# Kernel optimization log

Measured on AMD Instinct MI355X. Metric: run time of the kernel, lower is better.

Reference implementation:

```python
import jax, jax.numpy as jnp
import numpy as np

B, L1, V, E, H, Z = 16, 257, 32000, 256, 256, 256


def _lstm_layer(x, Wih, Whh, bih, bhh):
    # x: [B, T, E_in]; PyTorch gate order i, f, g, o
    b, H_ = x.shape[0], Whh.shape[1]

    def step(carry, xt):
        h, c = carry
        gates = xt @ Wih.T + h @ Whh.T + (bih + bhh)
        i, f, g, o = jnp.split(gates, 4, axis=-1)
        c = jax.nn.sigmoid(f) * c + jax.nn.sigmoid(i) * jnp.tanh(g)
        h = jax.nn.sigmoid(o) * jnp.tanh(c)
        return (h, c), h

    h0 = jnp.zeros((b, H_), x.dtype)
    _, hs = jax.lax.scan(step, (h0, h0), jnp.swapaxes(x, 0, 1))
    return jnp.swapaxes(hs, 0, 1)  # [B, T, H]


def setup_inputs() -> dict:
    key = jax.random.key(0)
    ks = jax.random.split(key, 16)
    s = 1.0 / np.sqrt(H)
    inp = {
        "z": jax.random.normal(ks[0], (B, Z), jnp.float32),
        "target_seq": jax.random.randint(ks[1], (B, L1), 0, V),
        "emb": jax.random.normal(ks[2], (V, E), jnp.float32) * 0.02,
        "Wg": jax.random.normal(ks[3], (H, Z), jnp.float32) * s,
        "bg": jax.random.normal(ks[4], (H,), jnp.float32) * s,
        "Wb": jax.random.normal(ks[5], (H, Z), jnp.float32) * s,
        "bb": jax.random.normal(ks[6], (H,), jnp.float32) * s,
        "W_ih0": jax.random.normal(ks[7], (4 * H, E), jnp.float32) * s,
        "W_hh0": jax.random.normal(ks[8], (4 * H, H), jnp.float32) * s,
        "b_ih0": jax.random.normal(ks[9], (4 * H,), jnp.float32) * s,
        "b_hh0": jax.random.normal(ks[10], (4 * H,), jnp.float32) * s,
        "W_ih1": jax.random.normal(ks[11], (4 * H, H), jnp.float32) * s,
        "W_hh1": jax.random.normal(ks[12], (4 * H, H), jnp.float32) * s,
        "b_ih1": jax.random.normal(ks[13], (4 * H,), jnp.float32) * s,
        "b_hh1": jax.random.normal(ks[14], (4 * H,), jnp.float32) * s,
        "W_out": jax.random.normal(ks[15], (V, H), jnp.float32) * s,
        "b_out": jnp.zeros((V,), jnp.float32),
    }
    return inp


def reference(z, target_seq, emb, Wg, bg, Wb, bb, W_ih0, W_hh0, b_ih0, b_hh0,
              W_ih1, W_hh1, b_ih1, b_hh1, W_out, b_out):
    # Teacher-forcing branch (eval mode: dropout = identity).
    emb_t = emb.at[0].set(0.0)  # padding_idx=0
    gamma = (z @ Wg.T + bg)[:, None, :]  # [B,1,H]
    beta = (z @ Wb.T + bb)[:, None, :]
    x = emb_t[target_seq[:, :-1]]  # [B, L, E]
    h1 = _lstm_layer(x, W_ih0, W_hh0, b_ih0, b_hh0)
    h2 = _lstm_layer(h1, W_ih1, W_hh1, b_ih1, b_hh1)
    filmed = gamma * h2 + beta  # [B, L, H]
    logits = filmed @ W_out.T + b_out  # [B, L, V]
    return logits
```

## Files before the change

### kernel.cpp

```cpp
#include <hip/hip_runtime.h>
#include <stdint.h>


#define B_  16
#define T_  256
#define H_  256
#define V_  32000
#define G4  1024

#define LTPB 512
#define FSTR 32

typedef unsigned short u16;
typedef unsigned long long u64;
typedef __attribute__((ext_vector_type(8))) short  short8;
typedef __attribute__((ext_vector_type(4))) short  short4v;
typedef __attribute__((ext_vector_type(4))) float  f32x4;

static __device__ __forceinline__ float bf2f(u16 u) {
  uint32_t i = ((uint32_t)u) << 16;
  return __builtin_bit_cast(float, i);
}
static __device__ __forceinline__ u16 f2bf(float f) {
  uint32_t i = __builtin_bit_cast(uint32_t, f);
  uint32_t lsb = (i >> 16) & 1u;
  i += 0x7fffu + lsb;
  return (u16)(i >> 16);
}
static __device__ __forceinline__ float sigf(float x) {
  return 1.0f / (1.0f + __expf(-x));
}
static __device__ __forceinline__ float tanhfast(float x) {
  return 1.0f - 2.0f / (1.0f + __expf(2.0f * x));
}

static __device__ __forceinline__ uint32_t f32_to_e4m3(float f) {
  uint32_t u = __builtin_bit_cast(uint32_t, f);
  uint32_t s = (u >> 24) & 0x80u;
  uint32_t mag = u & 0x7fffffffu;
  if (mag >= 0x43E00000u) return s | 0x7Eu;
  if (mag < 0x3C800000u) {
    float af = __builtin_bit_cast(float, mag);
    int q = (int)rintf(af * 512.0f);
    if (q >= 8) return s | 0x08u;
    return s | (uint32_t)q;
  }
  uint32_t lsb = (mag >> 20) & 1u;
  mag += 0x7ffffu + lsb;
  int e = (int)(mag >> 23) - 120;
  uint32_t m3 = (mag >> 20) & 7u;
  if (e >= 16) return s | 0x7Eu;
  return s | ((uint32_t)e << 3) | m3;
}


__global__ void k_convert(const float* __restrict__ src, u16* __restrict__ dst, int n) {
  int i = blockIdx.x * blockDim.x + threadIdx.x;
  int stride = gridDim.x * blockDim.x;
  for (; i < n; i += stride) dst[i] = f2bf(src[i]);
}

__global__ void k_addbias(const float* __restrict__ a, const float* __restrict__ b,
                          float* __restrict__ dst, int n) {
  int i = blockIdx.x * blockDim.x + threadIdx.x;
  if (i < n) dst[i] = a[i] + b[i];
}

__global__ void k_zeroi(int* __restrict__ p, int n) {
  int i = blockIdx.x * blockDim.x + threadIdx.x;
  if (i < n) p[i] = 0;
}

__global__ void k_packWg(const float* __restrict__ Whh, u16* __restrict__ pk) {
  int i = blockIdx.x * blockDim.x + threadIdx.x;
  int lane = i & 63;
  int fb = (i >> 6) & 15;
  int w  = i >> 10;
  int cb = fb >> 3, ks = fb & 7;
  int row = 512 + w * 32 + cb * 16 + (lane & 15);
  int kb  = ks * 32 + (lane >> 4) * 8;
  const float* src = Whh + (size_t)row * 256 + kb;
  short8 v;
  #pragma unroll
  for (int j = 0; j < 8; j++) v[j] = (short)f2bf(src[j]);
  *(short8*)(pk + (size_t)i * 8) = v;
}

__global__ void k_packW8(const float* __restrict__ Whh, u64* __restrict__ pk) {
  int i = blockIdx.x * blockDim.x + threadIdx.x;
  int lane = i & 63;
  int fo = (i >> 6) % 48;
  int w  = (i >> 6) / 48;
  int g8 = fo >> 4, cb = (fo >> 3) & 1, ks = fo & 7;
  int base = (g8 == 0) ? 0 : (g8 == 1 ? 256 : 768);
  int row = base + w * 32 + cb * 16 + (lane & 15);
  int kb  = ks * 32 + (lane >> 4) * 8;
  const float* src = Whh + (size_t)row * 256 + kb;
  u64 p = 0;
  #pragma unroll
  for (int j = 0; j < 8; j++)
    p |= ((u64)f32_to_e4m3(src[j])) << (8 * j);
  pk[i] = p;
}

__global__ void k_film(const float* __restrict__ z,
                       const float* __restrict__ Wg, const float* __restrict__ bg,
                       const float* __restrict__ Wb, const float* __restrict__ bb,
                       float* __restrict__ gamma, float* __restrict__ beta) {
  int tid = blockIdx.x * blockDim.x + threadIdx.x;
  int which = tid >> 12;
  int o = tid & 4095;
  int b = o >> 8, h = o & 255;
  const float* W  = which ? Wb : Wg;
  const float* bi = which ? bb : bg;
  float acc = bi[h];
  const float* zr = z + b * 256;
  const float* wr = W + h * 256;
  #pragma unroll 8
  for (int k = 0; k < 256; k++) acc += zr[k] * wr[k];
  (which ? beta : gamma)[o] = acc;
}

__global__ void k_gather(const int* __restrict__ seq, const float* __restrict__ emb,
                         u16* __restrict__ xb) {
  int i = blockIdx.x * blockDim.x + threadIdx.x;
  int n = B_ * T_ * (H_ / 4);
  if (i >= n) return;
  int e4 = i & 63;
  int bt = i >> 6;
  int t = bt & 255, b = bt >> 8;
  int row = seq[b * 257 + t];
  short4v p;
  if (row == 0) {
    p[0] = 0; p[1] = 0; p[2] = 0; p[3] = 0;
  } else {
    const f32x4 v = *(const f32x4*)(emb + (size_t)row * 256 + e4 * 4);
    p[0] = (short)f2bf(v[0]); p[1] = (short)f2bf(v[1]);
    p[2] = (short)f2bf(v[2]); p[3] = (short)f2bf(v[3]);
  }
  *(short4v*)(xb + (size_t)bt * 256 + e4 * 4) = p;
}


__global__ __launch_bounds__(256) void k_gemm_bt(
    const u16* __restrict__ A, const u16* __restrict__ Bm,
    const float* __restrict__ bias, float* __restrict__ C,
    int M, int N, int K, int permX) {
  __shared__ u16 sA[128 * 40];
  __shared__ u16 sB[128 * 40];
  const int tid  = threadIdx.x;
  const int lane = tid & 63;
  const int wv   = tid >> 6;
  const int wr   = wv >> 1, wc = wv & 1;
  const int m0 = blockIdx.y * 128, n0 = blockIdx.x * 128;
  const int rr = tid >> 2;
  const int cc = (tid & 3) * 8;

  f32x4 acc[4][4];
  #pragma unroll
  for (int m = 0; m < 4; m++)
    #pragma unroll
    for (int n = 0; n < 4; n++) acc[m][n] = (f32x4){0.f, 0.f, 0.f, 0.f};

  for (int ks = 0; ks < K; ks += 32) {
    short8 va0 = *(const short8*)(A  + (size_t)(m0 + rr)      * K + ks + cc);
    short8 va1 = *(const short8*)(A  + (size_t)(m0 + rr + 64) * K + ks + cc);
    short8 vb0 = *(const short8*)(Bm + (size_t)(n0 + rr)      * K + ks + cc);
    short8 vb1 = *(const short8*)(Bm + (size_t)(n0 + rr + 64) * K + ks + cc);
    __syncthreads();
    *(short8*)&sA[(rr)      * 40 + cc] = va0;
    *(short8*)&sA[(rr + 64) * 40 + cc] = va1;
    *(short8*)&sB[(rr)      * 40 + cc] = vb0;
    *(short8*)&sB[(rr + 64) * 40 + cc] = vb1;
    __syncthreads();
    const int kc = (lane >> 4) * 8;
    short8 af[4], bfr[4];
    #pragma unroll
    for (int m = 0; m < 4; m++)
      af[m] = *(const short8*)&sA[(wr * 64 + m * 16 + (lane & 15)) * 40 + kc];
    #pragma unroll
    for (int n = 0; n < 4; n++)
      bfr[n] = *(const short8*)&sB[(wc * 64 + n * 16 + (lane & 15)) * 40 + kc];
    #pragma unroll
    for (int m = 0; m < 4; m++)
      #pragma unroll
      for (int n = 0; n < 4; n++)
        acc[m][n] = __builtin_amdgcn_mfma_f32_16x16x32_bf16(af[m], bfr[n], acc[m][n], 0, 0, 0);
  }

  #pragma unroll
  for (int m = 0; m < 4; m++) {
    int row = m0 + wr * 64 + m * 16 + ((lane >> 4) << 2);
    #pragma unroll
    for (int n = 0; n < 4; n++) {
      int col = n0 + wc * 64 + n * 16 + (lane & 15);
      float bv = bias[col];
      int ocol = col;
      if (permX) {
        int g = col >> 8, r = col & 255;
        ocol = (r >> 5) * 128 + (r & 15) * 8 + g * 2 + ((r >> 4) & 1);
      }
      #pragma unroll
      for (int i = 0; i < 4; i++)
        C[(size_t)(row + i) * N + ocol] = acc[m][n][i] + bv;
    }
  }
}


static __device__ __forceinline__ void lstm_role(
    const float* __restrict__ Xpre, const u16* __restrict__ WpkG,
    const u64* __restrict__ Wpk8, u16* __restrict__ outb,
    const float* __restrict__ gamma, const float* __restrict__ beta,
    int mode, int s, int* flagOut, const int* flagIn,
    u16 (*hbuf)[256], u64 (*h8buf)[32]) {
  const int tid  = threadIdx.x;
  const int lane = tid & 63;
  const int w    = tid >> 6;
  const int l15  = lane & 15;
  const int lhi  = lane >> 4;

  short8 wgm[16];
  {
    const u16* bp = WpkG + ((size_t)(w * 16) * 64 + lane) * 8;
    #pragma unroll
    for (int f = 0; f < 16; ++f)
      wgm[f] = *(const short8*)(bp + (size_t)f * 512);
  }
  u64 w8r[48];
  {
    const u64* p8 = Wpk8 + (size_t)(w * 48) * 64 + lane;
    #pragma unroll
    for (int f = 0; f < 48; ++f)
      w8r[f] = p8[(size_t)f * 64];
  }

  const int col0 = w * 32 + l15;
  const int col1 = col0 + 16;
  float cs0 = 0.f, cs1 = 0.f;
  float gm0 = 1.f, gm1 = 1.f, bt0 = 0.f, bt1 = 0.f;
  if (mode) {
    gm0 = gamma[s * 256 + col0]; bt0 = beta[s * 256 + col0];
    gm1 = gamma[s * 256 + col1]; bt1 = beta[s * 256 + col1];
  }

  if (flagIn) {
    if (tid == 0) {
      while (__hip_atomic_load(flagIn, __ATOMIC_RELAXED,
                               __HIP_MEMORY_SCOPE_AGENT) < 1) { }
    }
    __syncthreads();
    __builtin_amdgcn_fence(__ATOMIC_ACQUIRE, "agent");
  }

  const float* xptr = Xpre + (size_t)s * T_ * 1024 + (size_t)(w * 16 + l15) * 8;

  f32x4 xa = *(const f32x4*)(xptr);
  f32x4 xg = *(const f32x4*)(xptr + 4);
  {
    float cn0 = sigf(xa[2]) * cs0 + sigf(xa[0]) * tanhfast(xg[0]);
    float hn0 = sigf(xg[2]) * tanhfast(cn0);
    cs0 = cn0;
    float cn1 = sigf(xa[3]) * cs1 + sigf(xa[1]) * tanhfast(xg[1]);
    float hn1 = sigf(xg[3]) * tanhfast(cn1);
    cs1 = cn1;
    u16 h0 = f2bf(hn0), h1 = f2bf(hn1);
    if (lhi == 0) {
      hbuf[0][col0] = h0;
      hbuf[0][col1] = h1;
      ((uint8_t*)h8buf[0])[col0] = (uint8_t)f32_to_e4m3(hn0);
      ((uint8_t*)h8buf[0])[col1] = (uint8_t)f32_to_e4m3(hn1);
      outb[(size_t)(s * T_) * 256 + col0] = mode ? f2bf(gm0 * hn0 + bt0) : h0;
      outb[(size_t)(s * T_) * 256 + col1] = mode ? f2bf(gm1 * hn1 + bt1) : h1;
    }
  }
  asm volatile("s_waitcnt lgkmcnt(0)" ::: "memory");
  __builtin_amdgcn_sched_barrier(0);
  __builtin_amdgcn_s_barrier();
  __builtin_amdgcn_sched_barrier(0);

  xa = *(const f32x4*)(xptr + 1024);
  xg = *(const f32x4*)(xptr + 1024 + 4);

  for (int t = 1; t < T_; ++t) {
    if (flagIn && (t & 15) == 15 && (t + 1) < T_) {
      const int need = ((t + 1) >> 4) + 1;
      if (tid == 0) {
        while (__hip_atomic_load(flagIn, __ATOMIC_RELAXED,
                                 __HIP_MEMORY_SCOPE_AGENT) < need) { }
      }
      __syncthreads();
      __builtin_amdgcn_fence(__ATOMIC_ACQUIRE, "agent");
    }

    const float* xn = xptr + (size_t)((t + 1 < T_) ? t + 1 : t) * 1024;
    f32x4 na = *(const f32x4*)(xn);
    f32x4 ng = *(const f32x4*)(xn + 4);

    const u16* hrd  = hbuf[(t + 1) & 1];
    const u64* h8rd = h8buf[(t + 1) & 1];

    f32x4 aI[2], aF[2], aG[2], aO[2];
    #pragma unroll
    for (int i = 0; i < 2; ++i) {
      aI[i] = (f32x4){0.f, 0.f, 0.f, 0.f};
      aF[i] = (f32x4){0.f, 0.f, 0.f, 0.f};
      aG[i] = (f32x4){0.f, 0.f, 0.f, 0.f};
      aO[i] = (f32x4){0.f, 0.f, 0.f, 0.f};
    }
    #pragma unroll
    for (int ks = 0; ks < 8; ++ks) {
      short8 a  = *(const short8*)&hrd[ks * 32 + lhi * 8];
      u64    a8 = h8rd[ks * 4 + lhi];
      aG[0] = __builtin_amdgcn_mfma_f32_16x16x32_bf16(a, wgm[ks],     aG[0], 0, 0, 0);
      aG[1] = __builtin_amdgcn_mfma_f32_16x16x32_bf16(a, wgm[8 + ks], aG[1], 0, 0, 0);
      aI[0] = __builtin_amdgcn_mfma_f32_16x16x32_fp8_fp8((long)a8, (long)w8r[ks],      aI[0], 0, 0, 0);
      aI[1] = __builtin_amdgcn_mfma_f32_16x16x32_fp8_fp8((long)a8, (long)w8r[8 + ks],  aI[1], 0, 0, 0);
      aF[0] = __builtin_amdgcn_mfma_f32_16x16x32_fp8_fp8((long)a8, (long)w8r[16 + ks], aF[0], 0, 0, 0);
      aF[1] = __builtin_amdgcn_mfma_f32_16x16x32_fp8_fp8((long)a8, (long)w8r[24 + ks], aF[1], 0, 0, 0);
      aO[0] = __builtin_amdgcn_mfma_f32_16x16x32_fp8_fp8((long)a8, (long)w8r[32 + ks], aO[0], 0, 0, 0);
      aO[1] = __builtin_amdgcn_mfma_f32_16x16x32_fp8_fp8((long)a8, (long)w8r[40 + ks], aO[1], 0, 0, 0);
    }

    float iv0 = aI[0][0] + xa[0], iv1 = aI[1][0] + xa[1];
    float fv0 = aF[0][0] + xa[2], fv1 = aF[1][0] + xa[3];
    float gv0 = aG[0][0] + xg[0], gv1 = aG[1][0] + xg[1];
    float ov0 = aO[0][0] + xg[2], ov1 = aO[1][0] + xg[3];

    float cn0 = sigf(fv0) * cs0 + sigf(iv0) * tanhfast(gv0);
    float hn0 = sigf(ov0) * tanhfast(cn0);
    cs0 = cn0;
    float cn1 = sigf(fv1) * cs1 + sigf(iv1) * tanhfast(gv1);
    float hn1 = sigf(ov1) * tanhfast(cn1);
    cs1 = cn1;

    u16 h0 = f2bf(hn0), h1 = f2bf(hn1);
    if (lhi == 0) {
      hbuf[t & 1][col0] = h0;
      hbuf[t & 1][col1] = h1;
      ((uint8_t*)h8buf[t & 1])[col0] = (uint8_t)f32_to_e4m3(hn0);
      ((uint8_t*)h8buf[t & 1])[col1] = (uint8_t)f32_to_e4m3(hn1);
      outb[((size_t)(s * T_ + t)) * 256 + col0] = mode ? f2bf(gm0 * hn0 + bt0) : h0;
      outb[((size_t)(s * T_ + t)) * 256 + col1] = mode ? f2bf(gm1 * hn1 + bt1) : h1;
    }

    if (flagOut && (t & 15) == 15) {
      __syncthreads();
      if (tid == 0) {
        __builtin_amdgcn_fence(__ATOMIC_RELEASE, "agent");
        __hip_atomic_store(flagOut, t + 1, __ATOMIC_RELAXED,
                           __HIP_MEMORY_SCOPE_AGENT);
      }
    } else {
      asm volatile("s_waitcnt lgkmcnt(0)" ::: "memory");
      __builtin_amdgcn_sched_barrier(0);
      __builtin_amdgcn_s_barrier();
      __builtin_amdgcn_sched_barrier(0);
    }

    xa = na;
    xg = ng;
  }
}

static __device__ __forceinline__ void xg_role(
    const u16* __restrict__ h1b, const u16* __restrict__ Wih1b,
    const float* __restrict__ b11, float* __restrict__ X1,
    int s, const int* flagA, int* flagB) {
  const int tid  = threadIdx.x;
  const int lane = tid & 63;
  const int w    = tid >> 6;
  const int l15  = lane & 15;
  const int lhi  = lane >> 4;

  for (int tc = 0; tc < 16; ++tc) {
    const int need = (tc + 1) * 16;
    if (tid == 0) {
      while (__hip_atomic_load(flagA, __ATOMIC_RELAXED,
                               __HIP_MEMORY_SCOPE_AGENT) < need) { }
    }
    __syncthreads();
    __builtin_amdgcn_fence(__ATOMIC_ACQUIRE, "agent");

    const int t0 = tc * 16;
    short8 afr[8];
    #pragma unroll
    for (int ks = 0; ks < 8; ++ks)
      afr[ks] = *(const short8*)(h1b + ((size_t)(s * T_ + t0 + l15)) * 256 + ks * 32 + lhi * 8);

    #pragma unroll
    for (int nt = 0; nt < 8; ++nt) {
      const int colb = w * 128 + nt * 16 + l15;
      f32x4 acc = (f32x4){0.f, 0.f, 0.f, 0.f};
      const u16* bp = Wih1b + (size_t)colb * 256 + lhi * 8;
      #pragma unroll
      for (int ks = 0; ks < 8; ++ks) {
        short8 bf = *(const short8*)(bp + ks * 32);
        acc = __builtin_amdgcn_mfma_f32_16x16x32_bf16(afr[ks], bf, acc, 0, 0, 0);
      }
      const int g = colb >> 8, r = colb & 255;
      const int ocol = (r >> 5) * 128 + (r & 15) * 8 + g * 2 + ((r >> 4) & 1);
      const float bv = b11[colb];
      #pragma unroll
      for (int i = 0; i < 4; ++i) {
        int trow = t0 + lhi * 4 + i;
        X1[((size_t)(s * T_ + trow)) * 1024 + ocol] = acc[i] + bv;
      }
    }

    __syncthreads();
    if (tid == 0) {
      __builtin_amdgcn_fence(__ATOMIC_RELEASE, "agent");
      __hip_atomic_store(flagB, tc + 1, __ATOMIC_RELAXED,
                         __HIP_MEMORY_SCOPE_AGENT);
    }
  }
}

__global__ __launch_bounds__(LTPB, 2) void k_fused(
    const float* __restrict__ X0, float* __restrict__ X1,
    const u16* __restrict__ WpG0, const u64* __restrict__ Wp80,
    const u16* __restrict__ WpG1, const u64* __restrict__ Wp81,
    const u16* __restrict__ Wih1b, const float* __restrict__ b11,
    u16* __restrict__ h1b, u16* __restrict__ filmb,
    const float* __restrict__ gamma, const float* __restrict__ beta,
    int* __restrict__ flagA, int* __restrict__ flagB) {
  __shared__ u16 hbuf[2][256];
  __shared__ u64 h8buf[2][32];
  const int role = blockIdx.x >> 4;
  const int s    = blockIdx.x & 15;
  if (role == 0) {
    lstm_role(X0, WpG0, Wp80, h1b, gamma, beta, 0, s,
              &flagA[s * FSTR], nullptr, hbuf, h8buf);
  } else if (role == 1) {
    xg_role(h1b, Wih1b, b11, X1, s, &flagA[s * FSTR], &flagB[s * FSTR]);
  } else {
    lstm_role(X1, WpG1, Wp81, filmb, gamma, beta, 1, s,
              nullptr, &flagB[s * FSTR], hbuf, h8buf);
  }
}


extern "C" void kernel_launch(void* const* d_in, const int* in_sizes, int n_in,
                              void* d_out, int out_size, void* d_ws, size_t ws_size,
                              hipStream_t stream) {
  const float* z    = (const float*)d_in[0];
  const int*   seq  = (const int*)  d_in[1];
  const float* emb  = (const float*)d_in[2];
  const float* Wg   = (const float*)d_in[3];
  const float* bg   = (const float*)d_in[4];
  const float* Wb   = (const float*)d_in[5];
  const float* bb   = (const float*)d_in[6];
  const float* Wih0 = (const float*)d_in[7];
  const float* Whh0 = (const float*)d_in[8];
  const float* bih0 = (const float*)d_in[9];
  const float* bhh0 = (const float*)d_in[10];
  const float* Wih1 = (const float*)d_in[11];
  const float* Whh1 = (const float*)d_in[12];
  const float* bih1 = (const float*)d_in[13];
  const float* bhh1 = (const float*)d_in[14];
  const float* Wout = (const float*)d_in[15];
  const float* bout = (const float*)d_in[16];

  char* ws = (char*)d_ws;
  size_t off = 0;
  auto take = [&](size_t bytes) -> char* {
    char* p = ws + off;
    off = (off + bytes + 255) & ~(size_t)255;
    return p;
  };
  float* gamma  = (float*)take(B_ * H_ * 4);
  float* beta   = (float*)take(B_ * H_ * 4);
  float* b01    = (float*)take(G4 * 4);
  float* b11    = (float*)take(G4 * 4);
  u16*   Wih0b  = (u16*)  take((size_t)G4 * H_ * 2);
  u16*   Wih1b  = (u16*)  take((size_t)G4 * H_ * 2);
  u16*   WpG0   = (u16*)  take((size_t)8 * 16 * 64 * 8 * 2);
  u64*   Wp80   = (u64*)  take((size_t)8 * 48 * 64 * 8);
  u16*   WpG1   = (u16*)  take((size_t)8 * 16 * 64 * 8 * 2);
  u64*   Wp81   = (u64*)  take((size_t)8 * 48 * 64 * 8);
  u16*   Woutb  = (u16*)  take((size_t)V_ * H_ * 2);
  u16*   xb     = (u16*)  take((size_t)B_ * T_ * H_ * 2);
  float* X0     = (float*)take((size_t)B_ * T_ * G4 * 4);
  float* X1     = (float*)take((size_t)B_ * T_ * G4 * 4);
  u16*   h1b    = (u16*)  take((size_t)B_ * T_ * H_ * 2);
  u16*   filmb  = (u16*)  take((size_t)B_ * T_ * H_ * 2);
  int*   flagA  = (int*)  take(B_ * FSTR * 4);
  int*   flagB  = (int*)  take(B_ * FSTR * 4);
  (void)ws_size; (void)in_sizes; (void)n_in; (void)out_size;

  k_convert<<<256, 256, 0, stream>>>(Wih0, Wih0b, G4 * H_);
  k_convert<<<256, 256, 0, stream>>>(Wih1, Wih1b, G4 * H_);
  k_convert<<<1024, 256, 0, stream>>>(Wout, Woutb, V_ * H_);
  k_packWg<<<32, 256, 0, stream>>>(Whh0, WpG0);
  k_packW8<<<96, 256, 0, stream>>>(Whh0, Wp80);
  k_packWg<<<32, 256, 0, stream>>>(Whh1, WpG1);
  k_packW8<<<96, 256, 0, stream>>>(Whh1, Wp81);
  k_addbias<<<4, 256, 0, stream>>>(bih0, bhh0, b01, G4);
  k_addbias<<<4, 256, 0, stream>>>(bih1, bhh1, b11, G4);
  k_zeroi<<<4, 256, 0, stream>>>(flagA, 2 * B_ * FSTR);
  k_film<<<32, 256, 0, stream>>>(z, Wg, bg, Wb, bb, gamma, beta);
  k_gather<<<1024, 256, 0, stream>>>(seq, emb, xb);

  k_gemm_bt<<<dim3(G4 / 128, (B_ * T_) / 128), 256, 0, stream>>>(
      xb, Wih0b, b01, X0, B_ * T_, G4, H_, 1);

  k_fused<<<48, LTPB, 0, stream>>>(X0, X1, WpG0, Wp80, WpG1, Wp81,
                                   Wih1b, b11, h1b, filmb, gamma, beta,
                                   flagA, flagB);

  k_gemm_bt<<<dim3(V_ / 128, (B_ * T_) / 128), 256, 0, stream>>>(
      filmb, Woutb, bout, (float*)d_out, B_ * T_, V_, H_, 0);
}
```

Measured before the change: 746.6 us.

## Fuse input projection and vocab GEMM into persistent pipelined LSTM kernel

Removes the two standalone GEMM launches. The layer-0 input projection and the vocabulary projection now run as extra roles inside the fused persistent kernel, linked to the LSTM roles through per-sequence flags. The vocab blocks spin on layer-1 progress and compute 64-row by 128-column output tiles as soon as the filmed hidden states are ready, so the large output GEMM overlaps the sequential recurrence. This relies on all 512 blocks being co-resident, because of the spin-waits. The vocab tile is smaller than the old 128x128 GEMM tile and the B operand is loaded straight from global memory, which may lower GEMM efficiency.

```diff
diff --git a/kernel.cpp b/kernel.cpp
--- a/kernel.cpp
+++ b/kernel.cpp
@@ -10,6 +10,8 @@
 
 #define LTPB 512
 #define FSTR 32
+#define NVW  448
+#define SASTR 264
 
 typedef unsigned short u16;
 typedef unsigned long long u64;
@@ -139,72 +141,6 @@
     p[2] = (short)f2bf(v[2]); p[3] = (short)f2bf(v[3]);
   }
   *(short4v*)(xb + (size_t)bt * 256 + e4 * 4) = p;
-}
-
-
-__global__ __launch_bounds__(256) void k_gemm_bt(
-    const u16* __restrict__ A, const u16* __restrict__ Bm,
-    const float* __restrict__ bias, float* __restrict__ C,
-    int M, int N, int K, int permX) {
-  __shared__ u16 sA[128 * 40];
-  __shared__ u16 sB[128 * 40];
-  const int tid  = threadIdx.x;
-  const int lane = tid & 63;
-  const int wv   = tid >> 6;
-  const int wr   = wv >> 1, wc = wv & 1;
-  const int m0 = blockIdx.y * 128, n0 = blockIdx.x * 128;
-  const int rr = tid >> 2;
-  const int cc = (tid & 3) * 8;
-
-  f32x4 acc[4][4];
-  #pragma unroll
-  for (int m = 0; m < 4; m++)
-    #pragma unroll
-    for (int n = 0; n < 4; n++) acc[m][n] = (f32x4){0.f, 0.f, 0.f, 0.f};
-
-  for (int ks = 0; ks < K; ks += 32) {
-    short8 va0 = *(const short8*)(A  + (size_t)(m0 + rr)      * K + ks + cc);
-    short8 va1 = *(const short8*)(A  + (size_t)(m0 + rr + 64) * K + ks + cc);
-    short8 vb0 = *(const short8*)(Bm + (size_t)(n0 + rr)      * K + ks + cc);
-    short8 vb1 = *(const short8*)(Bm + (size_t)(n0 + rr + 64) * K + ks + cc);
-    __syncthreads();
-    *(short8*)&sA[(rr)      * 40 + cc] = va0;
-    *(short8*)&sA[(rr + 64) * 40 + cc] = va1;
-    *(short8*)&sB[(rr)      * 40 + cc] = vb0;
-    *(short8*)&sB[(rr + 64) * 40 + cc] = vb1;
-    __syncthreads();
-    const int kc = (lane >> 4) * 8;
-    short8 af[4], bfr[4];
-    #pragma unroll
-    for (int m = 0; m < 4; m++)
-      af[m] = *(const short8*)&sA[(wr * 64 + m * 16 + (lane & 15)) * 40 + kc];
-    #pragma unroll
-    for (int n = 0; n < 4; n++)
-      bfr[n] = *(const short8*)&sB[(wc * 64 + n * 16 + (lane & 15)) * 40 + kc];
-    #pragma unroll
-    for (int m = 0; m < 4; m++)
-      #pragma unroll
-      for (int n = 0; n < 4; n++)
-        acc[m][n] = __builtin_amdgcn_mfma_f32_16x16x32_bf16(af[m], bfr[n], acc[m][n], 0, 0, 0);
-  }
-
-  #pragma unroll
-  for (int m = 0; m < 4; m++) {
-    int row = m0 + wr * 64 + m * 16 + ((lane >> 4) << 2);
-    #pragma unroll
-    for (int n = 0; n < 4; n++) {
-      int col = n0 + wc * 64 + n * 16 + (lane & 15);
-      float bv = bias[col];
-      int ocol = col;
-      if (permX) {
-        int g = col >> 8, r = col & 255;
-        ocol = (r >> 5) * 128 + (r & 15) * 8 + g * 2 + ((r >> 4) & 1);
-      }
-      #pragma unroll
-      for (int i = 0; i < 4; i++)
-        C[(size_t)(row + i) * N + ocol] = acc[m][n][i] + bv;
-    }
-  }
 }
 
 
@@ -363,10 +299,10 @@
   }
 }
 
-static __device__ __forceinline__ void xg_role(
-    const u16* __restrict__ h1b, const u16* __restrict__ Wih1b,
-    const float* __restrict__ b11, float* __restrict__ X1,
-    int s, const int* flagA, int* flagB) {
+static __device__ __forceinline__ void proj_role(
+    const u16* __restrict__ src, const u16* __restrict__ Wb_,
+    const float* __restrict__ bias, float* __restrict__ dst,
+    int s, const int* flagIn, int* flagOut) {
   const int tid  = threadIdx.x;
   const int lane = tid & 63;
   const int w    = tid >> 6;
@@ -374,25 +310,27 @@
   const int lhi  = lane >> 4;
 
   for (int tc = 0; tc < 16; ++tc) {
-    const int need = (tc + 1) * 16;
-    if (tid == 0) {
-      while (__hip_atomic_load(flagA, __ATOMIC_RELAXED,
-                               __HIP_MEMORY_SCOPE_AGENT) < need) { }
-    }
-    __syncthreads();
-    __builtin_amdgcn_fence(__ATOMIC_ACQUIRE, "agent");
+    if (flagIn) {
+      const int need = (tc + 1) * 16;
+      if (tid == 0) {
+        while (__hip_atomic_load(flagIn, __ATOMIC_RELAXED,
+                                 __HIP_MEMORY_SCOPE_AGENT) < need) { }
+      }
+      __syncthreads();
+      __builtin_amdgcn_fence(__ATOMIC_ACQUIRE, "agent");
+    }
 
     const int t0 = tc * 16;
     short8 afr[8];
     #pragma unroll
     for (int ks = 0; ks < 8; ++ks)
-      afr[ks] = *(const short8*)(h1b + ((size_t)(s * T_ + t0 + l15)) * 256 + ks * 32 + lhi * 8);
+      afr[ks] = *(const short8*)(src + ((size_t)(s * T_ + t0 + l15)) * 256 + ks * 32 + lhi * 8);
 
     #pragma unroll
     for (int nt = 0; nt < 8; ++nt) {
       const int colb = w * 128 + nt * 16 + l15;
       f32x4 acc = (f32x4){0.f, 0.f, 0.f, 0.f};
-      const u16* bp = Wih1b + (size_t)colb * 256 + lhi * 8;
+      const u16* bp = Wb_ + (size_t)colb * 256 + lhi * 8;
       #pragma unroll
       for (int ks = 0; ks < 8; ++ks) {
         short8 bf = *(const short8*)(bp + ks * 32);
@@ -400,43 +338,116 @@
       }
       const int g = colb >> 8, r = colb & 255;
       const int ocol = (r >> 5) * 128 + (r & 15) * 8 + g * 2 + ((r >> 4) & 1);
-      const float bv = b11[colb];
+      const float bv = bias[colb];
       #pragma unroll
       for (int i = 0; i < 4; ++i) {
         int trow = t0 + lhi * 4 + i;
-        X1[((size_t)(s * T_ + trow)) * 1024 + ocol] = acc[i] + bv;
+        dst[((size_t)(s * T_ + trow)) * 1024 + ocol] = acc[i] + bv;
       }
     }
 
     __syncthreads();
     if (tid == 0) {
       __builtin_amdgcn_fence(__ATOMIC_RELEASE, "agent");
-      __hip_atomic_store(flagB, tc + 1, __ATOMIC_RELAXED,
+      __hip_atomic_store(flagOut, tc + 1, __ATOMIC_RELAXED,
                          __HIP_MEMORY_SCOPE_AGENT);
     }
   }
 }
 
+static __device__ __forceinline__ void vocab_role(
+    const u16* __restrict__ filmb, const u16* __restrict__ Wo,
+    const float* __restrict__ bout, float* __restrict__ out,
+    const int* __restrict__ flagC, int wid, u16* __restrict__ sA) {
+  const int tid  = threadIdx.x;
+  const int lane = tid & 63;
+  const int w    = tid >> 6;
+  const int l15  = lane & 15;
+  const int lhi  = lane >> 4;
+
+  for (int n = wid; n < 16000; n += NVW) {
+    const int q   = n / 4000;
+    const int rem = n - q * 4000;
+    const int s   = rem / 250;
+    const int nt  = rem - s * 250;
+    const int need = q * 64 + 64;
+    if (tid == 0) {
+      while (__hip_atomic_load(&flagC[s * FSTR], __ATOMIC_RELAXED,
+                               __HIP_MEMORY_SCOPE_AGENT) < need) { }
+    }
+    __syncthreads();
+    __builtin_amdgcn_fence(__ATOMIC_ACQUIRE, "agent");
+
+    const int m0 = s * 256 + q * 64;
+    const int n0 = nt * 128;
+
+    {
+      const int r = tid >> 3, c = tid & 7;
+      const u16* srow = filmb + (size_t)(m0 + r) * 256 + c * 8;
+      #pragma unroll
+      for (int it = 0; it < 4; ++it)
+        *(short8*)&sA[r * SASTR + c * 8 + it * 64] = *(const short8*)(srow + it * 64);
+    }
+    __syncthreads();
+
+    const int colb = n0 + w * 16 + l15;
+    short8 bfr[8];
+    #pragma unroll
+    for (int ks = 0; ks < 8; ++ks)
+      bfr[ks] = *(const short8*)(Wo + (size_t)colb * 256 + ks * 32 + lhi * 8);
+
+    f32x4 acc[4];
+    #pragma unroll
+    for (int mi = 0; mi < 4; ++mi) acc[mi] = (f32x4){0.f, 0.f, 0.f, 0.f};
+    #pragma unroll
+    for (int ks = 0; ks < 8; ++ks) {
+      #pragma unroll
+      for (int mi = 0; mi < 4; ++mi) {
+        short8 a = *(const short8*)&sA[(mi * 16 + l15) * SASTR + ks * 32 + lhi * 8];
+        acc[mi] = __builtin_amdgcn_mfma_f32_16x16x32_bf16(a, bfr[ks], acc[mi], 0, 0, 0);
+      }
+    }
+
+    const float bv = bout[colb];
+    #pragma unroll
+    for (int mi = 0; mi < 4; ++mi)
+      #pragma unroll
+      for (int i = 0; i < 4; ++i)
+        out[(size_t)(m0 + mi * 16 + lhi * 4 + i) * V_ + colb] = acc[mi][i] + bv;
+  }
+}
+
 __global__ __launch_bounds__(LTPB, 2) void k_fused(
-    const float* __restrict__ X0, float* __restrict__ X1,
+    const u16* __restrict__ xb, float* __restrict__ X0, float* __restrict__ X1,
     const u16* __restrict__ WpG0, const u64* __restrict__ Wp80,
     const u16* __restrict__ WpG1, const u64* __restrict__ Wp81,
+    const u16* __restrict__ Wih0b, const float* __restrict__ b01,
     const u16* __restrict__ Wih1b, const float* __restrict__ b11,
-    u16* __restrict__ h1b, u16* __restrict__ filmb,
+    const u16* __restrict__ Woutb, const float* __restrict__ bout,
+    u16* __restrict__ h1b, u16* __restrict__ filmb, float* __restrict__ out,
     const float* __restrict__ gamma, const float* __restrict__ beta,
-    int* __restrict__ flagA, int* __restrict__ flagB) {
+    int* __restrict__ flagX, int* __restrict__ flagA,
+    int* __restrict__ flagB, int* __restrict__ flagC) {
   __shared__ u16 hbuf[2][256];
   __shared__ u64 h8buf[2][32];
-  const int role = blockIdx.x >> 4;
-  const int s    = blockIdx.x & 15;
-  if (role == 0) {
+  __shared__ u16 sA[64 * SASTR];
+
+  const int bid = blockIdx.x;
+  if (bid < 16) {
+    proj_role(xb, Wih0b, b01, X0, bid, nullptr, &flagX[bid * FSTR]);
+  } else if (bid < 32) {
+    const int s = bid - 16;
     lstm_role(X0, WpG0, Wp80, h1b, gamma, beta, 0, s,
-              &flagA[s * FSTR], nullptr, hbuf, h8buf);
-  } else if (role == 1) {
-    xg_role(h1b, Wih1b, b11, X1, s, &flagA[s * FSTR], &flagB[s * FSTR]);
+              &flagA[s * FSTR], &flagX[s * FSTR], hbuf, h8buf);
+  } else if (bid < 48) {
+    const int s = bid - 32;
+    proj_role(h1b, Wih1b, b11, X1, s, &flagA[s * FSTR], &flagB[s * FSTR]);
+  } else if (bid < 64) {
+    const int s = bid - 48;
+    lstm_role(X1, WpG1, Wp81, filmb, gamma, beta, 1, s,
+              &flagC[s * FSTR], &flagB[s * FSTR], hbuf, h8buf);
   } else {
-    lstm_role(X1, WpG1, Wp81, filmb, gamma, beta, 1, s,
-              nullptr, &flagB[s * FSTR], hbuf, h8buf);
+    vocab_role(filmb, Woutb, bout, out, flagC, bid - 64, sA);
   }
 }
 
@@ -485,8 +496,10 @@
   float* X1     = (float*)take((size_t)B_ * T_ * G4 * 4);
   u16*   h1b    = (u16*)  take((size_t)B_ * T_ * H_ * 2);
   u16*   filmb  = (u16*)  take((size_t)B_ * T_ * H_ * 2);
+  int*   flagX  = (int*)  take(B_ * FSTR * 4);
   int*   flagA  = (int*)  take(B_ * FSTR * 4);
   int*   flagB  = (int*)  take(B_ * FSTR * 4);
+  int*   flagC  = (int*)  take(B_ * FSTR * 4);
   (void)ws_size; (void)in_sizes; (void)n_in; (void)out_size;
 
   k_convert<<<256, 256, 0, stream>>>(Wih0, Wih0b, G4 * H_);
@@ -498,17 +511,12 @@
   k_packW8<<<96, 256, 0, stream>>>(Whh1, Wp81);
   k_addbias<<<4, 256, 0, stream>>>(bih0, bhh0, b01, G4);
   k_addbias<<<4, 256, 0, stream>>>(bih1, bhh1, b11, G4);
-  k_zeroi<<<4, 256, 0, stream>>>(flagA, 2 * B_ * FSTR);
+  k_zeroi<<<8, 256, 0, stream>>>(flagX, 4 * B_ * FSTR);
   k_film<<<32, 256, 0, stream>>>(z, Wg, bg, Wb, bb, gamma, beta);
   k_gather<<<1024, 256, 0, stream>>>(seq, emb, xb);
 
-  k_gemm_bt<<<dim3(G4 / 128, (B_ * T_) / 128), 256, 0, stream>>>(
-      xb, Wih0b, b01, X0, B_ * T_, G4, H_, 1);
-
-  k_fused<<<48, LTPB, 0, stream>>>(X0, X1, WpG0, Wp80, WpG1, Wp81,
-                                   Wih1b, b11, h1b, filmb, gamma, beta,
-                                   flagA, flagB);
-
-  k_gemm_bt<<<dim3(V_ / 128, (B_ * T_) / 128), 256, 0, stream>>>(
-      filmb, Woutb, bout, (float*)d_out, B_ * T_, V_, H_, 0);
-}
+  k_fused<<<64 + NVW, LTPB, 0, stream>>>(
+      xb, X0, X1, WpG0, Wp80, WpG1, Wp81, Wih0b, b01, Wih1b, b11,
+      Woutb, bout, h1b, filmb, (float*)d_out, gamma, beta,
+      flagX, flagA, flagB, flagC);
+}
```

Measured after the change: 1.376 ms. 1.84x slower.
